# Kernel tuning notes

Measured on AMD Instinct MI355X. Metric: run time of the kernel, lower is better.

Reference implementation:

```python
import math
import jax, jax.numpy as jnp
import numpy as np

jax.config.update("jax_enable_x64", True)

NUM_HEADS = 4
D_INNER = 256
D_STATE = 256
HEADDIM = D_INNER // NUM_HEADS
NUM_GRAPHS = 8
L_NODES = 512
N_NODES = NUM_GRAPHS * L_NODES
N_EDGES = 65536
TOL = 0.05  # self.tol


def dag_inverse(A, n):
    # Doubling Neumann series: (I+A)(I+A^2)(I+A^4)... = sum_{k<2^ceil(log2 n)} A^k
    # equals (I - A)^{-1} when A is nilpotent (DAG with diameter <= n).
    j = 2 ** math.ceil(math.log2(n))
    I = jnp.eye(A.shape[-1], dtype=A.dtype)
    last = A
    out = I + A
    for _ in range(2, int(math.log2(j)) + 1):
        last = last @ last
        out = out @ (I + last)
    return out


def _forward(x, Bmat, Cmat, dt, dt_edge, dt_bias, D, edge_index, data_batch, diameter):
    Bg, L, H, Hd = NUM_GRAPHS, L_NODES, NUM_HEADS, HEADDIM
    N = x.shape[0]
    # nodes are sorted by graph with equal graph sizes -> local index within graph
    local = jnp.arange(N) - data_batch * L

    def to_dense(v):  # (N, ...) -> (Bg, L, ...), equivalent of to_dense_batch
        return jnp.zeros((Bg, L) + v.shape[1:], v.dtype).at[data_batch, local].set(v)

    x_r = to_dense(x).reshape(Bg, L, H, Hd).transpose(0, 2, 1, 3)  # b n l h
    B_b = jnp.broadcast_to(to_dense(Bmat)[:, None], (Bg, H, L, D_STATE))  # broadcast_bc_in_heads
    C_b = jnp.broadcast_to(to_dense(Cmat)[:, None], (Bg, H, L, D_STATE))

    dt3 = dt.reshape(N, H, 4).transpose(2, 1, 0)  # 'l (n c) -> c n l'
    dt_self_d = to_dense(dt3[3].T).transpose(0, 2, 1)  # (b, n, l)

    def mul_dt_A(d):
        # A_log is a zeros buffer (with_A=False) -> A = -exp(0) = -1
        return -jax.nn.softplus(d + dt_bias[None, :, None])

    dt_A_node = mul_dt_A(dt3[:3])  # (3, n, N)
    dt_A_edge = mul_dt_A(dt_edge.reshape(-1, H, 1).transpose(2, 1, 0))  # (1, n, E)

    src, dst = edge_index[0], edge_index[1]
    dt_A = (dt_A_node[0][:, src] + dt_A_node[1][:, dst] + dt_A_edge[0]) / 3.0  # (n, E)
    vals = jnp.exp(dt_A).T  # (E, n)
    # to_dense_adj: scatter-add edge attrs into dense (b, l1, l2, n)
    adj = jnp.zeros((Bg, L, L, H), vals.dtype).at[
        data_batch[src], local[src], local[dst]].add(vals)
    adj = adj.transpose(0, 3, 1, 2)  # (b, n, l1, l2)

    dt_dummy = to_dense(jnp.exp(dt_A_node[2]).T).transpose(0, 2, 1)  # (b, n, l)
    # normalize_mat('sum_leq', sub_constraint='max')
    normalizer = jnp.maximum(1.0, adj.sum(-1) + dt_dummy)
    A_mat = adj / (normalizer[..., None] + TOL)

    # I_minus_A: fp64 doubling inverse of (I - A^T)
    Lm = dag_inverse(jnp.swapaxes(A_mat.astype(jnp.float64), -1, -2), diameter)
    Lm = Lm.astype(x.dtype)
    L_norm = Lm * dt_self_d[:, :, None, :]  # L * dt_self.unsqueeze(-2)

    y = jnp.einsum('bnld,bnlt,bntd,bnth->bnlh', C_b, L_norm, B_b, x_r)
    y = y + x_r * D[None, :, None, None]
    y = y.transpose(0, 2, 3, 1).reshape(Bg, L, Hd * H)  # 'b n l h -> b l (h n)'
    return y.reshape(N, Hd * H)  # mask is all-True (equal-size graphs)


def setup_inputs():
    key = jax.random.key(0)
    ks = jax.random.split(key, 8)
    x = jax.random.normal(ks[0], (N_NODES, D_INNER), dtype=jnp.float32)
    Bmat = jax.random.normal(ks[1], (N_NODES, D_STATE), dtype=jnp.float32)
    Cmat = jax.random.normal(ks[2], (N_NODES, D_STATE), dtype=jnp.float32)
    dt = jax.random.normal(ks[3], (N_NODES, NUM_HEADS * 4), dtype=jnp.float32)
    dt_edge = jax.random.normal(ks[4], (N_EDGES, NUM_HEADS), dtype=jnp.float32)
    per_graph = N_EDGES // NUM_GRAPHS
    g = jnp.repeat(jnp.arange(NUM_GRAPHS), per_graph)
    src = g * L_NODES + jax.random.randint(ks[5], (N_EDGES,), 0, L_NODES)
    dst = g * L_NODES + jax.random.randint(ks[6], (N_EDGES,), 0, L_NODES)
    edge_index = jnp.stack([src, dst]).astype(jnp.int32)
    data_batch = jnp.repeat(jnp.arange(NUM_GRAPHS), L_NODES).astype(jnp.int32)
    # dt_bias init as in module __init__
    dt_min, dt_max = 1e-3, 1e-1
    u = jax.random.uniform(ks[7], (NUM_HEADS,))
    dtv = jnp.exp(u * (math.log(dt_max) - math.log(dt_min)) + math.log(dt_min))
    dtv = jnp.clip(dtv, 1e-4, None)
    dt_bias = (dtv + jnp.log(-jnp.expm1(-dtv))).astype(jnp.float32)
    D = jnp.ones((NUM_HEADS,), dtype=jnp.float32)
    return {"x": x, "Bmat": Bmat, "Cmat": Cmat, "dt": dt, "dt_edge": dt_edge,
            "dt_bias": dt_bias, "D": D, "edge_index": edge_index,
            "data_batch": data_batch, "diameter": 32}


def reference(x, Bmat, Cmat, dt, dt_edge, dt_bias, D, edge_index, data_batch, diameter):
    return _forward(x, Bmat, Cmat, dt, dt_edge, dt_bias, D, edge_index, data_batch, diameter)
```

## Files before the change

kernel.cpp:

```cpp
#include <hip/hip_runtime.h>
#include <math.h>

#define N_EDGES 65536
#define LNODE 512
#define DSTATE 256
#define DINNER 256
#define HEADD 64

using bf16x8 = __attribute__((ext_vector_type(8))) short;
using f32x4  = __attribute__((ext_vector_type(4))) float;
using us4    = __attribute__((ext_vector_type(4))) unsigned short;
using us8    = __attribute__((ext_vector_type(8))) unsigned short;

__device__ __forceinline__ float softplusf(float z) {
  return (z > 0.0f) ? (z + log1pf(expf(-z))) : log1pf(expf(z));
}
__device__ __forceinline__ float bf2f(unsigned short u) {
  unsigned int x = ((unsigned int)u) << 16;
  return __builtin_bit_cast(float, x);
}
__device__ __forceinline__ unsigned short f2bf(float f) {
  unsigned int x = __builtin_bit_cast(unsigned int, f);
  x += 0x7fffu + ((x >> 16) & 1u);
  return (unsigned short)(x >> 16);
}

__global__ __launch_bounds__(256) void zero_ws_kernel(float* __restrict__ G,
                                                      float* __restrict__ colsum) {
  const size_t i = (size_t)blockIdx.x * 256 + threadIdx.x;
  const float4 z = make_float4(0.0f, 0.0f, 0.0f, 0.0f);
  if (i < 2097152) {
    ((float4*)G)[i] = z;
  } else {
    ((float4*)colsum)[i - 2097152] = z;
  }
}

__global__ void scatter_edges_kernel(const float* __restrict__ dt,
                                     const float* __restrict__ dt_edge,
                                     const float* __restrict__ dt_bias,
                                     const int* __restrict__ edge_index,
                                     float* __restrict__ G,
                                     float* __restrict__ colsum) {
  int t = blockIdx.x * blockDim.x + threadIdx.x;
  if (t >= N_EDGES * 4) return;
  int e = t >> 2;
  int n = t & 3;
  int src = edge_index[e];
  int dst = edge_index[N_EDGES + e];
  float bias = dt_bias[n];
  float z0 = dt[src * 16 + n * 4 + 0] + bias;
  float z1 = dt[dst * 16 + n * 4 + 1] + bias;
  float z2 = dt_edge[e * 4 + n] + bias;
  float val = expf(-(softplusf(z0) + softplusf(z1) + softplusf(z2)) * (1.0f / 3.0f));
  int b = src >> 9;
  int l1 = src & 511;
  int l2 = dst & 511;
  int bn = b * 4 + n;
  atomicAdd(&G[(((size_t)bn) << 18) + ((size_t)l2 << 9) + l1], val);
  atomicAdd(&colsum[bn * 512 + l1], val);
}

__global__ __launch_bounds__(256) void conv_kernel(const float* __restrict__ G,
                                                   const float* __restrict__ colsum,
                                                   const float* __restrict__ dt,
                                                   const float* __restrict__ dt_bias,
                                                   unsigned short* __restrict__ Prm,
                                                   unsigned short* __restrict__ Pt,
                                                   unsigned short* __restrict__ Q) {
  const int bn = blockIdx.y;
  const int n = bn & 3, b = bn >> 2;
  const size_t base = (size_t)bn << 18;
  const int tile = blockIdx.x;
  const int ro = (tile >> 4) << 5;
  const int co = (tile & 15) << 5;
  __shared__ float lds[32][33];
  __shared__ float sinv[32];
  const int t = threadIdx.x;
  if (t < 32) {
    const int col = co + t;
    float ssum = colsum[bn * 512 + col];
    float bias = dt_bias[n];
    float dummy = expf(-softplusf(dt[(size_t)(b * 512 + col) * 16 + n * 4 + 2] + bias));
    float norm = fmaxf(1.0f, ssum + dummy);
    sinv[t] = 1.0f / (norm + 0.05f);
  }
  __syncthreads();
  const int tr = t >> 3;
  const int tc0 = (t & 7) << 2;
  float4 gv = *(const float4*)(G + base + (size_t)(ro + tr) * 512 + co + tc0);
  float vv[4] = {gv.x, gv.y, gv.z, gv.w};
  us4 p, q;
#pragma unroll
  for (int j = 0; j < 4; ++j) {
    vv[j] *= sinv[tc0 + j];
    p[j] = f2bf(vv[j]);
    float qq = vv[j] + (((ro + tr) == (co + tc0 + j)) ? 1.0f : 0.0f);
    q[j] = f2bf(qq);
    lds[tc0 + j][tr] = vv[j];
  }
  *(us4*)(Prm + base + (size_t)(ro + tr) * 512 + co + tc0) = p;
  *(us4*)(Q + base + (size_t)(ro + tr) * 512 + co + tc0) = q;
  __syncthreads();
  us4 pt;
#pragma unroll
  for (int j = 0; j < 4; ++j) pt[j] = f2bf(lds[tr][tc0 + j]);
  *(us4*)(Pt + base + (size_t)(co + tr) * 512 + ro + tc0) = pt;
}

__global__ __launch_bounds__(512, 2) void gemm_pair_kernel(
    const unsigned short* __restrict__ A0p, const unsigned short* __restrict__ B0p,
    unsigned short* __restrict__ C0rm, unsigned short* __restrict__ C0t,
    const unsigned short* __restrict__ Q0,
    const unsigned short* __restrict__ A1p, const unsigned short* __restrict__ B1p,
    unsigned short* __restrict__ C1rm, unsigned short* __restrict__ C1t,
    const unsigned short* __restrict__ Q1) {
  const int f = (blockIdx.z * gridDim.y + blockIdx.y) * gridDim.x + blockIdx.x;
  const int rres = f & 7;
  const int q = f >> 3;
  const int tile = q & 3;
  const int unit = ((q >> 2) << 3) + rres;
  const int bn = unit & 31;
  const int z = unit >> 5;

  const unsigned short* A    = z ? A1p : A0p;
  const unsigned short* Bt   = z ? B1p : B0p;
  unsigned short* Crm        = z ? C1rm : C0rm;
  unsigned short* Ct         = z ? C1t : C0t;
  const unsigned short* Qadd = z ? Q1 : Q0;

  const size_t off = (size_t)bn << 18;
  A += off; Bt += off;
  if (Crm) Crm += off;
  if (Ct) Ct += off;
  if (Qadd) Qadd += off;
  const int m0 = (tile >> 1) << 8;
  const int n0 = (tile & 1) << 8;

  __shared__ __align__(16) char lds[131072];
  const int tid = threadIdx.x;
  const int lane = tid & 63;
  const int wid = tid >> 6;
  const int wr = wid >> 2;
  const int wc = wid & 3;
  const int cl = lane & 15;
  const int kq = lane >> 4;
  const int rg = kq << 2;

  f32x4 acc[8][4];
#pragma unroll
  for (int i = 0; i < 8; ++i)
#pragma unroll
    for (int j = 0; j < 4; ++j) acc[i][j] = (f32x4)(0.0f);

  auto stage = [&](int db, int kt, int mat, int h) {
    const unsigned short* src = mat ? Bt : A;
    const int t0 = (mat ? n0 : m0) + h * 128;
    char* base = lds + db * 65536 + mat * 32768 + h * 16384;
#pragma unroll
    for (int s = 0; s < 2; ++s) {
      const int c = s * 512 + tid;
      const int r = c >> 3;
      const int ks = (c & 7) ^ (r & 7);
      const unsigned short* g = src + (size_t)(t0 + r) * 512 + kt * 64 + (ks << 3);
      __builtin_amdgcn_global_load_lds(
          (const __attribute__((address_space(1))) void*)g,
          (__attribute__((address_space(3))) void*)(base + c * 16),
          16, 0, 0);
    }
  };

  bf16x8 av[4][2];
  bf16x8 bv[4][2];

  auto readA = [&](int db, int mh) {
#pragma unroll
    for (int i = 0; i < 4; ++i) {
      const int r = i * 32 + wr * 16 + cl;
      const int rb = db * 65536 + mh * 16384 + r * 128;
      const int x = (r & 7);
#pragma unroll
      for (int kk = 0; kk < 2; ++kk)
        av[i][kk] = *(const bf16x8*)(lds + rb + (((kk * 4 + kq) ^ x) << 4));
    }
  };
  auto readB = [&](int db, int nh) {
#pragma unroll
    for (int j = 0; j < 2; ++j) {
      const int r = j * 64 + wc * 16 + cl;
      const int rb = db * 65536 + 32768 + nh * 16384 + r * 128;
      const int x = (r & 7);
#pragma unroll
      for (int kk = 0; kk < 2; ++kk)
        bv[nh * 2 + j][kk] = *(const bf16x8*)(lds + rb + (((kk * 4 + kq) ^ x) << 4));
    }
  };
  auto quad = [&](int mh, int nh) {
    __builtin_amdgcn_s_setprio(1);
#pragma unroll
    for (int i = 0; i < 4; ++i)
#pragma unroll
      for (int j = 0; j < 2; ++j)
#pragma unroll
        for (int kk = 0; kk < 2; ++kk)
          acc[mh * 4 + i][nh * 2 + j] = __builtin_amdgcn_mfma_f32_16x16x32_bf16(
              av[i][kk], bv[nh * 2 + j][kk], acc[mh * 4 + i][nh * 2 + j], 0, 0, 0);
    __builtin_amdgcn_s_setprio(0);
  };

  stage(0, 0, 0, 0); stage(0, 0, 1, 0); stage(0, 0, 1, 1); stage(0, 0, 0, 1);

#pragma unroll
  for (int kt = 0; kt < 8; ++kt) {
    const int db = kt & 1;
    if (kt < 7) {
      stage(db ^ 1, kt + 1, 0, 0);
      asm volatile("s_waitcnt vmcnt(6)" ::: "memory");
    } else {
      asm volatile("s_waitcnt vmcnt(4)" ::: "memory");
    }
    __builtin_amdgcn_s_barrier();
    readA(db, 0); readB(db, 0);
    asm volatile("s_waitcnt lgkmcnt(0)" ::: "memory");
    __builtin_amdgcn_sched_barrier(0);
    quad(0, 0);
    if (kt < 7) {
      stage(db ^ 1, kt + 1, 1, 0);
      asm volatile("s_waitcnt vmcnt(6)" ::: "memory");
    } else {
      asm volatile("s_waitcnt vmcnt(2)" ::: "memory");
    }
    __builtin_amdgcn_s_barrier();
    readB(db, 1);
    asm volatile("s_waitcnt lgkmcnt(0)" ::: "memory");
    __builtin_amdgcn_sched_barrier(0);
    quad(0, 1);
    if (kt < 7) {
      stage(db ^ 1, kt + 1, 1, 1);
      asm volatile("s_waitcnt vmcnt(6)" ::: "memory");
    } else {
      asm volatile("s_waitcnt vmcnt(0)" ::: "memory");
    }
    __builtin_amdgcn_s_barrier();
    readA(db, 1);
    asm volatile("s_waitcnt lgkmcnt(0)" ::: "memory");
    __builtin_amdgcn_sched_barrier(0);
    quad(1, 0);
    if (kt < 7) stage(db ^ 1, kt + 1, 0, 1);
    quad(1, 1);
    __builtin_amdgcn_sched_barrier(0);
  }

  unsigned short hreg[8][4][4];
#pragma unroll
  for (int mi = 0; mi < 8; ++mi) {
#pragma unroll
    for (int ni = 0; ni < 4; ++ni) {
      const int gr = m0 + mi * 32 + wr * 16 + rg;
      const int gc = n0 + ni * 64 + wc * 16 + cl;
      float v0 = acc[mi][ni][0], v1 = acc[mi][ni][1];
      float v2 = acc[mi][ni][2], v3 = acc[mi][ni][3];
      if (Qadd) {
        v0 += bf2f(Qadd[(size_t)(gr + 0) * 512 + gc]);
        v1 += bf2f(Qadd[(size_t)(gr + 1) * 512 + gc]);
        v2 += bf2f(Qadd[(size_t)(gr + 2) * 512 + gc]);
        v3 += bf2f(Qadd[(size_t)(gr + 3) * 512 + gc]);
      }
      unsigned short h0 = f2bf(v0), h1 = f2bf(v1), h2 = f2bf(v2), h3 = f2bf(v3);
      hreg[mi][ni][0] = h0; hreg[mi][ni][1] = h1;
      hreg[mi][ni][2] = h2; hreg[mi][ni][3] = h3;
      if (Crm) {
        Crm[(size_t)(gr + 0) * 512 + gc] = h0;
        Crm[(size_t)(gr + 1) * 512 + gc] = h1;
        Crm[(size_t)(gr + 2) * 512 + gc] = h2;
        Crm[(size_t)(gr + 3) * 512 + gc] = h3;
      }
    }
  }
  if (Ct) {
    unsigned short* tl = (unsigned short*)lds;
#pragma unroll
    for (int p = 0; p < 2; ++p) {
      __syncthreads();
#pragma unroll
      for (int mi = 0; mi < 8; ++mi)
#pragma unroll
        for (int j = 0; j < 2; ++j) {
          const int ni = p * 2 + j;
          const int lcol = j * 64 + wc * 16 + cl;
          const int lrow = mi * 32 + wr * 16 + rg;
          us4 v; v[0] = hreg[mi][ni][0]; v[1] = hreg[mi][ni][1];
          v[2] = hreg[mi][ni][2]; v[3] = hreg[mi][ni][3];
          *(us4*)(tl + lcol * 264 + lrow) = v;
        }
      __syncthreads();
      const int c = tid >> 2;
      const int q4 = tid & 3;
      const unsigned short* srcp = tl + c * 264 + q4 * 64;
      unsigned short* dstp = Ct + (size_t)(n0 + p * 128 + c) * 512 + m0 + q4 * 64;
#pragma unroll
      for (int u = 0; u < 8; ++u)
        *(us8*)(dstp + u * 8) = *(const us8*)(srcp + u * 8);
    }
  }
}

__global__ __launch_bounds__(256) void gemm_nt_kernel(const float* __restrict__ Cm,
                                                      const float* __restrict__ Bm,
                                                      float* __restrict__ S) {
  const int f = blockIdx.y * gridDim.x + blockIdx.x;
  const int b = f & 7;
  const int tile = f >> 3;
  const float* Ab = Cm + (size_t)b * LNODE * DSTATE;
  const float* Bb = Bm + (size_t)b * LNODE * DSTATE;
  float* Sb = S + ((size_t)b << 18);
  const int m0 = (tile >> 3) << 6;
  const int n0 = (tile & 7) << 6;
  __shared__ float As[16][68];
  __shared__ float Bs[16][68];
  const int tid = threadIdx.x;
  const int tx = tid & 15, ty = tid >> 4;
  const int srow = tid >> 2, skq = tid & 3;
  float acc[4][4] = {};
  for (int k0 = 0; k0 < DSTATE; k0 += 16) {
    float4 a = *(const float4*)(Ab + (size_t)(m0 + srow) * DSTATE + k0 + skq * 4);
    As[skq * 4 + 0][srow] = a.x; As[skq * 4 + 1][srow] = a.y;
    As[skq * 4 + 2][srow] = a.z; As[skq * 4 + 3][srow] = a.w;
    float4 c = *(const float4*)(Bb + (size_t)(n0 + srow) * DSTATE + k0 + skq * 4);
    Bs[skq * 4 + 0][srow] = c.x; Bs[skq * 4 + 1][srow] = c.y;
    Bs[skq * 4 + 2][srow] = c.z; Bs[skq * 4 + 3][srow] = c.w;
    __syncthreads();
#pragma unroll
    for (int k = 0; k < 16; ++k) {
      float av[4], bv[4];
      *(float4*)(av) = *(const float4*)(&As[k][ty * 4]);
      *(float4*)(bv) = *(const float4*)(&Bs[k][tx * 4]);
#pragma unroll
      for (int i = 0; i < 4; ++i)
#pragma unroll
        for (int j = 0; j < 4; ++j)
          acc[i][j] = fmaf(av[i], bv[j], acc[i][j]);
    }
    __syncthreads();
  }
#pragma unroll
  for (int i = 0; i < 4; ++i) {
    float* sp = Sb + (size_t)(m0 + ty * 4 + i) * 512 + n0 + tx * 4;
    *(float4*)sp = make_float4(acc[i][0], acc[i][1], acc[i][2], acc[i][3]);
  }
}

__global__ __launch_bounds__(256) void final_fused_kernel(
    const unsigned short* __restrict__ Lm, const float* __restrict__ S,
    const float* __restrict__ dt, const float* __restrict__ x,
    float* __restrict__ P) {
  const int f = (blockIdx.z * gridDim.y + blockIdx.y) * gridDim.x + blockIdx.x;
  const int rres = f & 7;
  const int q = f >> 3;
  const int sub = q & 15;
  const int bn = ((q >> 4) << 3) + rres;
  const int ltile = sub & 3;
  const int kg = sub >> 2;
  const int n = bn & 3, b = bn >> 2;
  const unsigned short* Lb = Lm + ((size_t)bn << 18);
  const float* Sb = S + ((size_t)b << 18);
  const float* xb = x + (size_t)b * LNODE * DINNER + n * HEADD;
  const int m0 = ltile << 7;
  const int kbase = kg << 7;
  __shared__ float Ms[16][132];
  __shared__ float Xs[16][64];
  __shared__ float dts_all[128];
  const int tid = threadIdx.x;
  const int tx = tid & 15, ty = tid >> 4;
  if (tid < 128)
    dts_all[tid] = dt[(size_t)(b * 512 + kbase + tid) * 16 + n * 4 + 3];
  __syncthreads();
  float acc[8][4] = {};
  for (int kk0 = 0; kk0 < 128; kk0 += 16) {
    const int k0 = kbase + kk0;
#pragma unroll
    for (int s = 0; s < 2; ++s) {
      int fid = tid + s * 256;
      int m = fid >> 2, kq = fid & 3;
      us4 lm = *(const us4*)(Lb + (size_t)(m0 + m) * 512 + k0 + kq * 4);
      float4 sv = *(const float4*)(Sb + (size_t)(m0 + m) * 512 + k0 + kq * 4);
      Ms[kq * 4 + 0][m] = bf2f(lm[0]) * sv.x * dts_all[kk0 + kq * 4 + 0];
      Ms[kq * 4 + 1][m] = bf2f(lm[1]) * sv.y * dts_all[kk0 + kq * 4 + 1];
      Ms[kq * 4 + 2][m] = bf2f(lm[2]) * sv.z * dts_all[kk0 + kq * 4 + 2];
      Ms[kq * 4 + 3][m] = bf2f(lm[3]) * sv.w * dts_all[kk0 + kq * 4 + 3];
    }
    {
      int kk = tid >> 4, hq = tid & 15;
      float4 v = *(const float4*)(xb + (size_t)(k0 + kk) * DINNER + hq * 4);
      *(float4*)(&Xs[kk][hq * 4]) = v;
    }
    __syncthreads();
#pragma unroll
    for (int k = 0; k < 16; ++k) {
      float mv[8], xv[4];
      *(float4*)(mv)     = *(const float4*)(&Ms[k][ty * 8]);
      *(float4*)(mv + 4) = *(const float4*)(&Ms[k][ty * 8 + 4]);
      *(float4*)(xv)     = *(const float4*)(&Xs[k][tx * 4]);
#pragma unroll
      for (int i = 0; i < 8; ++i)
#pragma unroll
        for (int j = 0; j < 4; ++j)
          acc[i][j] = fmaf(mv[i], xv[j], acc[i][j]);
    }
    __syncthreads();
  }
  float* Pb = P + (((size_t)(kg * 32 + bn)) << 15);
#pragma unroll
  for (int i = 0; i < 8; ++i) {
    const int l = m0 + ty * 8 + i;
    *(float4*)(Pb + (size_t)l * 64 + tx * 4) =
        make_float4(acc[i][0], acc[i][1], acc[i][2], acc[i][3]);
  }
}

__global__ __launch_bounds__(256) void reduce_out_kernel(
    const float* __restrict__ P, const float* __restrict__ x,
    const float* __restrict__ Dv, float* __restrict__ out) {
  int t = blockIdx.x * 256 + threadIdx.x;
  int h = t & 63;
  int l = (t >> 6) & 511;
  int b = t >> 15;
  float4 v;
#pragma unroll
  for (int n = 0; n < 4; ++n) {
    int bn = b * 4 + n;
    float s = 0.0f;
#pragma unroll
    for (int kg = 0; kg < 4; ++kg)
      s += P[(((size_t)(kg * 32 + bn)) << 15) + (size_t)l * 64 + h];
    s += x[(size_t)(b * 512 + l) * 256 + n * 64 + h] * Dv[n];
    ((float*)&v)[n] = s;
  }
  *(float4*)(out + (size_t)(b * 512 + l) * 256 + h * 4) = v;
}

extern "C" void kernel_launch(void* const* d_in, const int* in_sizes, int n_in,
                              void* d_out, int out_size, void* d_ws, size_t ws_size,
                              hipStream_t stream) {
  const float* x        = (const float*)d_in[0];
  const float* Bmat     = (const float*)d_in[1];
  const float* Cmat     = (const float*)d_in[2];
  const float* dt       = (const float*)d_in[3];
  const float* dt_edge  = (const float*)d_in[4];
  const float* dt_bias  = (const float*)d_in[5];
  const float* Dv       = (const float*)d_in[6];
  const int* edge_index = (const int*)d_in[7];
  float* out = (float*)d_out;

  char* wsb = (char*)d_ws;
  const size_t SL = 16777216;
  unsigned short* sA = (unsigned short*)(wsb + 0 * SL);
  unsigned short* sB = (unsigned short*)(wsb + 1 * SL);
  unsigned short* sC = (unsigned short*)(wsb + 2 * SL);
  unsigned short* sD = (unsigned short*)(wsb + 3 * SL);
  unsigned short* sE = (unsigned short*)(wsb + 4 * SL);
  unsigned short* sF = (unsigned short*)(wsb + 5 * SL);
  float* G      = (float*)(wsb + 3 * SL);
  float* Sbuf   = (float*)(wsb + 5 * SL);
  float* Pbuf   = (float*)(wsb + 3 * SL);
  float* colsum = (float*)(wsb + 6 * SL);

  zero_ws_kernel<<<8208, 256, 0, stream>>>(G, colsum);
  scatter_edges_kernel<<<1024, 256, 0, stream>>>(dt, dt_edge, dt_bias, edge_index, G, colsum);
  conv_kernel<<<dim3(256, 32), 256, 0, stream>>>(G, colsum, dt, dt_bias, sA, sB, sC);

  dim3 g1(4, 32, 1), g2(4, 32, 2);
  gemm_pair_kernel<<<g1, 512, 0, stream>>>(sA, sB, sD, sE, nullptr,
                                           nullptr, nullptr, nullptr, nullptr, nullptr);
  gemm_pair_kernel<<<g2, 512, 0, stream>>>(sD, sE, sA, sB, nullptr,
                                           sC, sE, sF, nullptr, sC);
  gemm_pair_kernel<<<g2, 512, 0, stream>>>(sA, sB, sC, sD, nullptr,
                                           sF, sB, sE, nullptr, sF);
  gemm_nt_kernel<<<dim3(64, 8), 256, 0, stream>>>(Cmat, Bmat, Sbuf);
  gemm_pair_kernel<<<g2, 512, 0, stream>>>(sC, sD, nullptr, sA, nullptr,
                                           sE, sD, sB, nullptr, sE);
  gemm_pair_kernel<<<g1, 512, 0, stream>>>(sB, sA, sC, nullptr, sB,
                                           nullptr, nullptr, nullptr, nullptr, nullptr);

  final_fused_kernel<<<dim3(4, 4, 32), 256, 0, stream>>>(sC, Sbuf, dt, x, Pbuf);
  reduce_out_kernel<<<1024, 256, 0, stream>>>(Pbuf, x, Dv, out);
}
```

Measured before the change: 240.7 us.

## Fuse the GEMM chain into one cooperative persistent kernel with grid syncs

Replaces the five separate gemm_pair_kernel launches of the doubling-inverse chain with a single cooperative kernel of 256 blocks that runs each stage and uses grid.sync between stages. Buffer assignments are remapped (colsum and Sbuf move, the final output lands in sB) so gemm_nt can run before the chain without aliasing. This removes kernel launch gaps and tail effects between stages. In exchange it adds grid-wide barriers and requires all 256 blocks of 512 threads with 128KB LDS to be co-resident, and it leaves half the blocks idle in the first and last stages.

```diff
diff --git a/kernel.cpp b/kernel.cpp
--- a/kernel.cpp
+++ b/kernel.cpp
@@ -1,5 +1,8 @@
 #include <hip/hip_runtime.h>
+#include <hip/hip_cooperative_groups.h>
 #include <math.h>
+
+namespace cg = cooperative_groups;
 
 #define N_EDGES 65536
 #define LNODE 512
@@ -108,27 +111,10 @@
   *(us4*)(Pt + base + (size_t)(co + tr) * 512 + ro + tc0) = pt;
 }
 
-__global__ __launch_bounds__(512, 2) void gemm_pair_kernel(
-    const unsigned short* __restrict__ A0p, const unsigned short* __restrict__ B0p,
-    unsigned short* __restrict__ C0rm, unsigned short* __restrict__ C0t,
-    const unsigned short* __restrict__ Q0,
-    const unsigned short* __restrict__ A1p, const unsigned short* __restrict__ B1p,
-    unsigned short* __restrict__ C1rm, unsigned short* __restrict__ C1t,
-    const unsigned short* __restrict__ Q1) {
-  const int f = (blockIdx.z * gridDim.y + blockIdx.y) * gridDim.x + blockIdx.x;
-  const int rres = f & 7;
-  const int q = f >> 3;
-  const int tile = q & 3;
-  const int unit = ((q >> 2) << 3) + rres;
-  const int bn = unit & 31;
-  const int z = unit >> 5;
-
-  const unsigned short* A    = z ? A1p : A0p;
-  const unsigned short* Bt   = z ? B1p : B0p;
-  unsigned short* Crm        = z ? C1rm : C0rm;
-  unsigned short* Ct         = z ? C1t : C0t;
-  const unsigned short* Qadd = z ? Q1 : Q0;
-
+__device__ __attribute__((always_inline)) inline void run_unit(
+    char* lds, const unsigned short* A, const unsigned short* Bt,
+    unsigned short* Crm, unsigned short* Ct, const unsigned short* Qadd,
+    int bn, int tile) {
   const size_t off = (size_t)bn << 18;
   A += off; Bt += off;
   if (Crm) Crm += off;
@@ -137,7 +123,6 @@
   const int m0 = (tile >> 1) << 8;
   const int n0 = (tile & 1) << 8;
 
-  __shared__ __align__(16) char lds[131072];
   const int tid = threadIdx.x;
   const int lane = tid & 63;
   const int wid = tid >> 6;
@@ -303,6 +288,41 @@
         *(us8*)(dstp + u * 8) = *(const us8*)(srcp + u * 8);
     }
   }
+}
+
+__device__ __forceinline__ void decode_unit(int ff, int& bn, int& tile, int& z) {
+  int rres = ff & 7, qq = ff >> 3;
+  tile = qq & 3;
+  int unit = ((qq >> 2) << 3) + rres;
+  bn = unit & 31;
+  z = unit >> 5;
+}
+
+__global__ __launch_bounds__(512, 2) void chain_coop_kernel(
+    unsigned short* sA, unsigned short* sB, unsigned short* sC,
+    unsigned short* sD, unsigned short* sE, unsigned short* sF) {
+  __shared__ __align__(16) char lds[131072];
+  cg::grid_group grid = cg::this_grid();
+  const int blk = blockIdx.x;
+  int bn, tile, z;
+  decode_unit(blk, bn, tile, z);
+
+  if (blk < 128) run_unit(lds, sA, sB, sD, sE, nullptr, bn, tile);
+  __threadfence(); grid.sync();
+
+  if (z == 0) run_unit(lds, sD, sE, sA, sB, nullptr, bn, tile);
+  else        run_unit(lds, sC, sE, sF, nullptr, sC, bn, tile);
+  __threadfence(); grid.sync();
+
+  if (z == 0) run_unit(lds, sA, sB, sD, sE, nullptr, bn, tile);
+  else        run_unit(lds, sF, sB, sC, nullptr, sF, bn, tile);
+  __threadfence(); grid.sync();
+
+  if (z == 0) run_unit(lds, sD, sE, nullptr, sA, nullptr, bn, tile);
+  else        run_unit(lds, sC, sE, sF, nullptr, sC, bn, tile);
+  __threadfence(); grid.sync();
+
+  if (blk < 128) run_unit(lds, sF, sA, sB, nullptr, sF, bn, tile);
 }
 
 __global__ __launch_bounds__(256) void gemm_nt_kernel(const float* __restrict__ Cm,
@@ -461,27 +481,20 @@
   unsigned short* sE = (unsigned short*)(wsb + 4 * SL);
   unsigned short* sF = (unsigned short*)(wsb + 5 * SL);
   float* G      = (float*)(wsb + 3 * SL);
-  float* Sbuf   = (float*)(wsb + 5 * SL);
+  float* colsum = (float*)(wsb + 5 * SL);
+  float* Sbuf   = (float*)(wsb + 6 * SL);
   float* Pbuf   = (float*)(wsb + 3 * SL);
-  float* colsum = (float*)(wsb + 6 * SL);
 
   zero_ws_kernel<<<8208, 256, 0, stream>>>(G, colsum);
   scatter_edges_kernel<<<1024, 256, 0, stream>>>(dt, dt_edge, dt_bias, edge_index, G, colsum);
   conv_kernel<<<dim3(256, 32), 256, 0, stream>>>(G, colsum, dt, dt_bias, sA, sB, sC);
-
-  dim3 g1(4, 32, 1), g2(4, 32, 2);
-  gemm_pair_kernel<<<g1, 512, 0, stream>>>(sA, sB, sD, sE, nullptr,
-                                           nullptr, nullptr, nullptr, nullptr, nullptr);
-  gemm_pair_kernel<<<g2, 512, 0, stream>>>(sD, sE, sA, sB, nullptr,
-                                           sC, sE, sF, nullptr, sC);
-  gemm_pair_kernel<<<g2, 512, 0, stream>>>(sA, sB, sC, sD, nullptr,
-                                           sF, sB, sE, nullptr, sF);
   gemm_nt_kernel<<<dim3(64, 8), 256, 0, stream>>>(Cmat, Bmat, Sbuf);
-  gemm_pair_kernel<<<g2, 512, 0, stream>>>(sC, sD, nullptr, sA, nullptr,
-                                           sE, sD, sB, nullptr, sE);
-  gemm_pair_kernel<<<g1, 512, 0, stream>>>(sB, sA, sC, nullptr, sB,
-                                           nullptr, nullptr, nullptr, nullptr, nullptr);
-
-  final_fused_kernel<<<dim3(4, 4, 32), 256, 0, stream>>>(sC, Sbuf, dt, x, Pbuf);
+
+  void* args[6] = {(void*)&sA, (void*)&sB, (void*)&sC,
+                   (void*)&sD, (void*)&sE, (void*)&sF};
+  hipLaunchCooperativeKernel(reinterpret_cast<void*>(chain_coop_kernel),
+                             dim3(256), dim3(512), args, 0, stream);
+
+  final_fused_kernel<<<dim3(4, 4, 32), 256, 0, stream>>>(sB, Sbuf, dt, x, Pbuf);
   reduce_out_kernel<<<1024, 256, 0, stream>>>(Pbuf, x, Dv, out);
 }
```

After: 691.6 us. +187.3%, slower.
